# Kernel tuning notes

Measured on AMD Instinct MI355X. Metric: run time of the kernel, lower is better.

Reference implementation:

```python
import jax, jax.numpy as jnp
import numpy as np

D_MODEL = 768
EXPAND = 2
D_INNER = EXPAND * D_MODEL  # 1536
D_STATE = 16
D_CONV = 4
DT_RANK = D_MODEL // 16  # 48
N_LAYER = 3
BATCH, SEQLEN = 2, 1024
EPS = 1e-5


def setup_inputs() -> dict:
    key = jax.random.key(0)
    ks = jax.random.split(key, 8)
    s = 0.02
    hidden_states = jax.random.normal(ks[0], (BATCH, SEQLEN, D_MODEL), jnp.float32)
    norm_w = jnp.ones((N_LAYER, D_MODEL), jnp.float32)
    in_proj_w = s * jax.random.normal(ks[1], (N_LAYER, 2 * D_INNER, D_MODEL), jnp.float32)
    conv_w = s * jax.random.normal(ks[2], (N_LAYER, D_INNER, D_CONV), jnp.float32)
    conv_b = jnp.zeros((N_LAYER, D_INNER), jnp.float32)
    x_proj_w = s * jax.random.normal(ks[3], (N_LAYER, DT_RANK + 2 * D_STATE, D_INNER), jnp.float32)
    dt_proj_w = s * jax.random.normal(ks[4], (N_LAYER, D_INNER, DT_RANK), jnp.float32)
    dt_proj_b = jnp.full((N_LAYER, D_INNER), -4.6, jnp.float32)  # softplus ~ 0.01
    # S4D-real init: A_log = log(1..d_state), tiled over channels
    A_log = jnp.tile(jnp.log(jnp.arange(1, D_STATE + 1, dtype=jnp.float32))[None, None, :], (N_LAYER, D_INNER, 1))
    D_skip = jnp.ones((N_LAYER, D_INNER), jnp.float32)
    out_proj_w = s * jax.random.normal(ks[5], (N_LAYER, D_MODEL, D_INNER), jnp.float32)
    norm_f_w = jnp.ones((D_MODEL,), jnp.float32)
    return dict(hidden_states=hidden_states, norm_w=norm_w, in_proj_w=in_proj_w,
                conv_w=conv_w, conv_b=conv_b, x_proj_w=x_proj_w, dt_proj_w=dt_proj_w,
                dt_proj_b=dt_proj_b, A_log=A_log, D_skip=D_skip, out_proj_w=out_proj_w,
                norm_f_w=norm_f_w)


def _rmsnorm(x, w):
    return x * jax.lax.rsqrt(jnp.mean(x * x, axis=-1, keepdims=True) + EPS) * w


def _causal_conv1d(x, w, b):
    # x: [B, L, D]; w: [D, K] depthwise; left-pad for causality
    xt = jnp.transpose(x, (0, 2, 1))  # [B, D, L]
    y = jax.lax.conv_general_dilated(xt, w[:, None, :], window_strides=(1,),
                                     padding=[(D_CONV - 1, 0)], feature_group_count=D_INNER)
    return jnp.transpose(y, (0, 2, 1)) + b


def _selective_scan(u, delta, A, Bc, Cc, Dp):
    # u, delta: [B, L, D]; A: [D, N]; Bc, Cc: [B, L, N]
    def step(h, inp):
        dt, bt, ct, ut = inp  # [B,D], [B,N], [B,N], [B,D]
        h = jnp.exp(dt[..., None] * A) * h + (dt * ut)[..., None] * bt[:, None, :]
        y = jnp.einsum('bdn,bn->bd', h, ct)
        return h, y
    h0 = jnp.zeros((u.shape[0], u.shape[2], A.shape[1]), u.dtype)
    xs = (jnp.swapaxes(delta, 0, 1), jnp.swapaxes(Bc, 0, 1), jnp.swapaxes(Cc, 0, 1), jnp.swapaxes(u, 0, 1))
    _, ys = jax.lax.scan(step, h0, xs)  # ys: [L, B, D]
    return jnp.swapaxes(ys, 0, 1) + u * Dp


def _mixer(h, in_w, cw, cb, xw, dtw, dtb, A_log, Dp, ow):
    xz = jnp.einsum('bld,ed->ble', h, in_w)  # [B, L, 2*D_INNER]
    x, z = xz[..., :D_INNER], xz[..., D_INNER:]
    x = jax.nn.silu(_causal_conv1d(x, cw, cb))
    x_dbl = jnp.einsum('bld,ed->ble', x, xw)
    dt = x_dbl[..., :DT_RANK]
    Bc = x_dbl[..., DT_RANK:DT_RANK + D_STATE]
    Cc = x_dbl[..., DT_RANK + D_STATE:]
    delta = jax.nn.softplus(jnp.einsum('blr,dr->bld', dt, dtw) + dtb)
    A = -jnp.exp(A_log)
    y = _selective_scan(x, delta, A, Bc, Cc, Dp)
    y = y * jax.nn.silu(z)
    return jnp.einsum('bld,ed->ble', y, ow)


def reference(hidden_states, norm_w, in_proj_w, conv_w, conv_b, x_proj_w, dt_proj_w,
              dt_proj_b, A_log, D_skip, out_proj_w, norm_f_w):
    hidden = hidden_states
    residual = None
    for i in range(N_LAYER):
        residual = hidden if residual is None else hidden + residual  # fused add
        hidden = _rmsnorm(residual, norm_w[i])
        hidden = _mixer(hidden, in_proj_w[i], conv_w[i], conv_b[i], x_proj_w[i],
                        dt_proj_w[i], dt_proj_b[i], A_log[i], D_skip[i], out_proj_w[i])
    # final fused add + RMSNorm (prenorm=False)
    return _rmsnorm(hidden + residual, norm_f_w)
```

## Files before the change

### kernel.cpp

```cpp
#include <hip/hip_runtime.h>
#include <math.h>

#define D_MODEL 768
#define D_INNER 1536
#define D_STATE 16
#define D_CONV 4
#define DT_RANK 48
#define N_LAYER 3
#define BATCH 2
#define SEQLEN 1024
#define NROWS (BATCH * SEQLEN)
#define XDBL_W (DT_RANK + 2 * D_STATE)
#define EPS 1e-5f

#define SCLEN 16
#define SDN 16
#define KSPLIT_X 8

typedef short bf16x8 __attribute__((ext_vector_type(8)));
typedef float f32x4 __attribute__((ext_vector_type(4)));

__device__ __forceinline__ ushort f2bf(float x) {
    union { float f; uint u; } v; v.f = x;
    uint r = v.u + 0x7fff + ((v.u >> 16) & 1);
    return (ushort)(r >> 16);
}

__device__ __forceinline__ void gload_lds16(const void* g, void* l) {
    __builtin_amdgcn_global_load_lds(
        (const __attribute__((address_space(1))) unsigned int*)g,
        (__attribute__((address_space(3))) unsigned int*)l, 16, 0, 0);
}

__global__ __launch_bounds__(256) void cvt_bf16_kernel(
    const float* __restrict__ s, ushort* __restrict__ d, int n4)
{
    int i = blockIdx.x * 256 + threadIdx.x;
    if (i >= n4) return;
    float4 v = ((const float4*)s)[i];
    ushort4 o;
    o.x = f2bf(v.x); o.y = f2bf(v.y); o.z = f2bf(v.z); o.w = f2bf(v.w);
    ((ushort4*)d)[i] = o;
}

__global__ __launch_bounds__(256) void cvt_xw_pad_kernel(
    const float* __restrict__ src, ushort* __restrict__ dst)
{
    const int per = 128 * 1536 / 4;
    int i = blockIdx.x * 256 + threadIdx.x;
    if (i >= 3 * per) return;
    int li = i / per, rem = i - li * per;
    int r = (rem * 4) / 1536, c = (rem * 4) % 1536;
    ushort4 o = make_ushort4(0, 0, 0, 0);
    if (r < XDBL_W) {
        const float* s = src + ((size_t)li * XDBL_W + r) * 1536 + c;
        o.x = f2bf(s[0]); o.y = f2bf(s[1]); o.z = f2bf(s[2]); o.w = f2bf(s[3]);
    }
    ((ushort4*)dst)[i] = o;
}

__global__ __launch_bounds__(256) void cvt_dtw_pad_kernel(
    const float* __restrict__ src, ushort* __restrict__ dst)
{
    const int per = 1536 * 64 / 4;
    int i = blockIdx.x * 256 + threadIdx.x;
    if (i >= 3 * per) return;
    int li = i / per, rem = i - li * per;
    int r = (rem * 4) / 64, c = (rem * 4) % 64;
    ushort4 o = make_ushort4(0, 0, 0, 0);
    if (c < DT_RANK) {
        const float* s = src + ((size_t)li * 1536 + r) * DT_RANK + c;
        o.x = f2bf(s[0]); o.y = f2bf(s[1]); o.z = f2bf(s[2]); o.w = f2bf(s[3]);
    }
    ((ushort4*)dst)[i] = o;
}

__global__ __launch_bounds__(256) void add_rmsnorm_kernel(
    const float* __restrict__ x, const float* __restrict__ res_in,
    const float* __restrict__ w, float* __restrict__ res_out,
    float* __restrict__ normed_f32, ushort* __restrict__ normed_bf)
{
    int row = blockIdx.x;
    int tid = threadIdx.x;
    const float* xr = x + row * D_MODEL;
    float v[3];
    float ss = 0.f;
#pragma unroll
    for (int i = 0; i < 3; i++) {
        int c = tid + i * 256;
        float t = xr[c];
        if (res_in) t += res_in[row * D_MODEL + c];
        v[i] = t;
        ss += t * t;
    }
    for (int off = 32; off; off >>= 1) ss += __shfl_xor(ss, off, 64);
    __shared__ float red[4];
    if ((tid & 63) == 0) red[tid >> 6] = ss;
    __syncthreads();
    float tot = red[0] + red[1] + red[2] + red[3];
    float scale = rsqrtf(tot * (1.f / D_MODEL) + EPS);
#pragma unroll
    for (int i = 0; i < 3; i++) {
        int c = tid + i * 256;
        if (res_out) res_out[row * D_MODEL + c] = v[i];
        float o = v[i] * scale * w[c];
        if (normed_f32) normed_f32[row * D_MODEL + c] = o;
        if (normed_bf)  normed_bf[row * D_MODEL + c] = f2bf(o);
    }
}

template <int BM, int BN, int EPI, int SPLITK>
__global__ __launch_bounds__(256) void gemm_mfma_kernel(
    const ushort* __restrict__ A, const ushort* __restrict__ W,
    const float* __restrict__ bias, float* __restrict__ C,
    int ldc, int Nout, int M, int K)
{
    constexpr int TM = BM / 32;
    constexpr int TN = BN / 32;
    __shared__ __attribute__((aligned(16))) ushort As[BM * 64];
    __shared__ __attribute__((aligned(16))) ushort Ws[BN * 64];
    const int t = threadIdx.x;
    const int lane = t & 63, w = t >> 6;
    const int ln15 = lane & 15, q = lane >> 4;
    const int row0 = blockIdx.y * BM, col0 = blockIdx.x * BN;
    const int wm0 = (w & 1) * (BM / 2), wn0 = (w >> 1) * (BN / 2);

    int kper = K / SPLITK;
    int kz = (SPLITK > 1) ? blockIdx.z * kper : 0;
    if (SPLITK > 1) C += (size_t)blockIdx.z * M * ldc;

    f32x4 acc[TM][TN];
#pragma unroll
    for (int i = 0; i < TM; i++)
#pragma unroll
        for (int j = 0; j < TN; j++) acc[i][j] = (f32x4){0.f, 0.f, 0.f, 0.f};

    for (int k0 = kz; k0 < kz + kper; k0 += 64) {
        __syncthreads();
#pragma unroll
        for (int i = 0; i < BM / 32; i++) {
            int p = (i * 4 + w) * 64 + lane;
            int r = p >> 3, s = p & 7;
            int g = s ^ (r & 7);
            gload_lds16(A + (size_t)(row0 + r) * K + k0 + g * 8, &As[p * 8]);
        }
#pragma unroll
        for (int i = 0; i < BN / 32; i++) {
            int p = (i * 4 + w) * 64 + lane;
            int r = p >> 3, s = p & 7;
            int g = s ^ (r & 7);
            gload_lds16(W + (size_t)(col0 + r) * K + k0 + g * 8, &Ws[p * 8]);
        }
        __syncthreads();
#pragma unroll
        for (int ks = 0; ks < 2; ks++) {
            bf16x8 af[TM], wf[TN];
#pragma unroll
            for (int im = 0; im < TM; im++) {
                int m = wm0 + im * 16 + ln15;
                int slot = (ks * 4 + q) ^ (m & 7);
                af[im] = *(const bf16x8*)&As[m * 64 + slot * 8];
            }
#pragma unroll
            for (int jn = 0; jn < TN; jn++) {
                int n = wn0 + jn * 16 + ln15;
                int slot = (ks * 4 + q) ^ (n & 7);
                wf[jn] = *(const bf16x8*)&Ws[n * 64 + slot * 8];
            }
#pragma unroll
            for (int im = 0; im < TM; im++)
#pragma unroll
                for (int jn = 0; jn < TN; jn++)
                    acc[im][jn] = __builtin_amdgcn_mfma_f32_16x16x32_bf16(
                        af[im], wf[jn], acc[im][jn], 0, 0, 0);
        }
    }
#pragma unroll
    for (int im = 0; im < TM; im++) {
#pragma unroll
        for (int jn = 0; jn < TN; jn++) {
            int rr = row0 + wm0 + im * 16 + q * 4;
            int cc = col0 + wn0 + jn * 16 + ln15;
            if (cc < Nout) {
                float* cp = C + (size_t)rr * ldc + cc;
#pragma unroll
                for (int r = 0; r < 4; r++) {
                    float v = acc[im][jn][r];
                    if (EPI == 1) {
                        v += bias[cc];
                        v = (v > 20.f) ? v : log1pf(__expf(v));
                    }
                    cp[(size_t)r * ldc] = v;
                }
            }
        }
    }
}

__global__ __launch_bounds__(256) void xreduce_kernel(
    const float* __restrict__ Cp, float* __restrict__ xdbl,
    ushort* __restrict__ xdt)
{
    const int S4 = NROWS * XDBL_W / 4;
    int i = blockIdx.x * 256 + threadIdx.x;
    if (i >= S4) return;
    const float4* p = (const float4*)Cp;
    float4 o = p[i];
#pragma unroll
    for (int z = 1; z < KSPLIT_X; z++) {
        float4 a = p[i + (size_t)z * S4];
        o.x += a.x; o.y += a.y; o.z += a.z; o.w += a.w;
    }
    ((float4*)xdbl)[i] = o;
    int row = (i * 4) / XDBL_W, c0 = (i * 4) % XDBL_W;
    if (c0 < DT_RANK) {
        ushort4 b;
        b.x = f2bf(o.x); b.y = f2bf(o.y); b.z = f2bf(o.z); b.w = f2bf(o.w);
        *(ushort4*)&xdt[(size_t)row * 64 + c0] = b;
    } else if (c0 < 64) {
        *(ushort4*)&xdt[(size_t)row * 64 + c0] = make_ushort4(0, 0, 0, 0);
    }
}

__global__ __launch_bounds__(256) void conv_silu_kernel(
    const float* __restrict__ xz, const float* __restrict__ cw,
    const float* __restrict__ cb, float* __restrict__ out,
    ushort* __restrict__ out_bf)
{
    int idx = blockIdx.x * 256 + threadIdx.x;
    int d = idx % D_INNER;
    int bl = idx / D_INNER;
    int l = bl % SEQLEN;
    float s = cb[d];
    const float* xp = xz + (size_t)bl * (2 * D_INNER) + d;
#pragma unroll
    for (int k = 0; k < D_CONV; k++) {
        int ls = l - (D_CONV - 1) + k;
        if (ls >= 0) s += cw[d * D_CONV + k] * xp[(k - (D_CONV - 1)) * (2 * D_INNER)];
    }
    float sil = s / (1.f + __expf(-s));
    out[(size_t)bl * D_INNER + d] = sil;
    out_bf[(size_t)bl * D_INNER + d] = f2bf(sil);
}

__global__ __launch_bounds__(1024) void scan2_kernel(
    const float* __restrict__ u, const float* __restrict__ delta,
    const float* __restrict__ A_log, const float* __restrict__ xdbl,
    const float* __restrict__ Dskip, const float* __restrict__ xz,
    ushort* __restrict__ ybf)
{
    __shared__ float PL[16][SDN * 17];
    __shared__ float HL[16][SDN * 17];
    const int t = threadIdx.x;
    const int lane = t & 63;
    const int w = t >> 6;
    const int dsub = lane & 15;
    const int csub = lane >> 4;
    const int c = w * 4 + csub;
    const int b = blockIdx.x / (D_INNER / SDN);
    const int d = (blockIdx.x % (D_INNER / SDN)) * SDN + dsub;

    float a2[D_STATE];
#pragma unroll
    for (int n = 0; n < D_STATE; n++)
        a2[n] = -__expf(A_log[d * D_STATE + n]) * 1.44269504f;

    const size_t base = (size_t)b * SEQLEN * D_INNER + d;
    const float* dtp = delta + base;
    const float* up  = u + base;
    const float* xrow = xdbl + (size_t)b * SEQLEN * XDBL_W;
    const int l0 = c * SCLEN;

    float h[D_STATE], P[D_STATE];
#pragma unroll
    for (int n = 0; n < D_STATE; n++) { h[n] = 0.f; P[n] = 1.f; }

    for (int i = 0; i < SCLEN; i++) {
        const int l = l0 + i;
        float dt = dtp[(size_t)l * D_INNER];
        float uu = up[(size_t)l * D_INNER];
        const float4* Bv = (const float4*)(xrow + (size_t)l * XDBL_W + DT_RANK);
        float4 q0 = Bv[0], q1 = Bv[1], q2 = Bv[2], q3 = Bv[3];
        float Bf[D_STATE] = {q0.x,q0.y,q0.z,q0.w, q1.x,q1.y,q1.z,q1.w,
                             q2.x,q2.y,q2.z,q2.w, q3.x,q3.y,q3.z,q3.w};
        float dtu = dt * uu;
#pragma unroll
        for (int n = 0; n < D_STATE; n++) {
            float e = __builtin_amdgcn_exp2f(dt * a2[n]);
            P[n] *= e;
            h[n] = e * h[n] + dtu * Bf[n];
        }
    }

#pragma unroll
    for (int n = 0; n < D_STATE; n++) {
        float Pp = __shfl(P[n], lane - 16, 64);
        float Hp = __shfl(h[n], lane - 16, 64);
        bool act = csub >= 1;
        h[n] = act ? P[n] * Hp + h[n] : h[n];
        P[n] = act ? P[n] * Pp : P[n];
    }
#pragma unroll
    for (int n = 0; n < D_STATE; n++) {
        float Pp = __shfl(P[n], lane - 32, 64);
        float Hp = __shfl(h[n], lane - 32, 64);
        bool act = csub >= 2;
        h[n] = act ? P[n] * Hp + h[n] : h[n];
        P[n] = act ? P[n] * Pp : P[n];
    }

    if (csub == 3) {
#pragma unroll
        for (int n = 0; n < D_STATE; n++) {
            PL[w][dsub * 17 + n] = P[n];
            HL[w][dsub * 17 + n] = h[n];
        }
    }
    __syncthreads();

    if (t < SDN * D_STATE) {
        const int d2 = t >> 4, n2 = t & 15;
        float hin = 0.f;
        for (int ww = 0; ww < 16; ww++) {
            float Pw = PL[ww][d2 * 17 + n2];
            float Hw = HL[ww][d2 * 17 + n2];
            HL[ww][d2 * 17 + n2] = hin;
            hin = Pw * hin + Hw;
        }
    }
    __syncthreads();

#pragma unroll
    for (int n = 0; n < D_STATE; n++) {
        float Win = HL[w][dsub * 17 + n];
        float Pe = __shfl(P[n], lane - 16, 64);
        float He = __shfl(h[n], lane - 16, 64);
        h[n] = (csub == 0) ? Win : Pe * Win + He;
    }

    const float Dsk = Dskip[d];
    const float* zp = xz + (size_t)b * SEQLEN * (2 * D_INNER) + D_INNER + d;
    ushort* yp = ybf + base;
    for (int i = 0; i < SCLEN; i++) {
        const int l = l0 + i;
        float dt = dtp[(size_t)l * D_INNER];
        float uu = up[(size_t)l * D_INNER];
        float zz = zp[(size_t)l * (2 * D_INNER)];
        const float4* Bv = (const float4*)(xrow + (size_t)l * XDBL_W + DT_RANK);
        float4 q0 = Bv[0], q1 = Bv[1], q2 = Bv[2], q3 = Bv[3];
        float4 r0 = Bv[4], r1 = Bv[5], r2 = Bv[6], r3 = Bv[7];
        float Bf[D_STATE] = {q0.x,q0.y,q0.z,q0.w, q1.x,q1.y,q1.z,q1.w,
                             q2.x,q2.y,q2.z,q2.w, q3.x,q3.y,q3.z,q3.w};
        float Cf[D_STATE] = {r0.x,r0.y,r0.z,r0.w, r1.x,r1.y,r1.z,r1.w,
                             r2.x,r2.y,r2.z,r2.w, r3.x,r3.y,r3.z,r3.w};
        float dtu = dt * uu;
        float acc = 0.f;
#pragma unroll
        for (int n = 0; n < D_STATE; n++) {
            float e = __builtin_amdgcn_exp2f(dt * a2[n]);
            h[n] = e * h[n] + dtu * Bf[n];
            acc += h[n] * Cf[n];
        }
        float yy = acc + uu * Dsk;
        float ee = __builtin_amdgcn_exp2f(-zz * 1.44269504f);
        float sil = zz * __builtin_amdgcn_rcpf(1.f + ee);
        yp[(size_t)l * D_INNER] = f2bf(yy * sil);
    }
}

extern "C" void kernel_launch(void* const* d_in, const int* in_sizes, int n_in,
                              void* d_out, int out_size, void* d_ws, size_t ws_size,
                              hipStream_t stream)
{
    const float* hs        = (const float*)d_in[0];
    const float* norm_w    = (const float*)d_in[1];
    const float* in_proj_w = (const float*)d_in[2];
    const float* conv_w    = (const float*)d_in[3];
    const float* conv_b    = (const float*)d_in[4];
    const float* x_proj_w  = (const float*)d_in[5];
    const float* dt_proj_w = (const float*)d_in[6];
    const float* dt_proj_b = (const float*)d_in[7];
    const float* A_log     = (const float*)d_in[8];
    const float* D_skip    = (const float*)d_in[9];
    const float* out_proj_w= (const float*)d_in[10];
    const float* norm_f_w  = (const float*)d_in[11];

    float* ws = (float*)d_ws;
    float* residual = ws;
    float* hidden   = residual + NROWS * D_MODEL;
    float* xz       = hidden + NROWS * D_MODEL;
    float* xconv    = xz + NROWS * 2 * D_INNER;
    float* xdbl     = xconv + NROWS * D_INNER;
    float* delta    = xdbl + NROWS * XDBL_W;
    float* xpart    = delta + NROWS * D_INNER;
    ushort* normbf  = (ushort*)(xpart + (size_t)KSPLIT_X * NROWS * XDBL_W);
    ushort* ybf     = normbf + NROWS * D_MODEL;
    ushort* xconvbf = ybf + NROWS * D_INNER;
    ushort* xdtbf   = xconvbf + NROWS * D_INNER;
    ushort* win_bf  = xdtbf + NROWS * 64;
    ushort* wout_bf = win_bf + (size_t)N_LAYER * 2 * D_INNER * D_MODEL;
    ushort* xw_pad  = wout_bf + (size_t)N_LAYER * D_MODEL * D_INNER;
    ushort* dtw_pad = xw_pad + (size_t)N_LAYER * 128 * 1536;

    {
        int n_in4  = N_LAYER * 2 * D_INNER * D_MODEL / 4;
        int n_out4 = N_LAYER * D_MODEL * D_INNER / 4;
        cvt_bf16_kernel<<<(n_in4 + 255) / 256, 256, 0, stream>>>(in_proj_w, win_bf, n_in4);
        cvt_bf16_kernel<<<(n_out4 + 255) / 256, 256, 0, stream>>>(out_proj_w, wout_bf, n_out4);
        cvt_xw_pad_kernel<<<(3 * 128 * 1536 / 4 + 255) / 256, 256, 0, stream>>>(x_proj_w, xw_pad);
        cvt_dtw_pad_kernel<<<(3 * 1536 * 64 / 4 + 255) / 256, 256, 0, stream>>>(dt_proj_w, dtw_pad);
    }

    for (int i = 0; i < N_LAYER; i++) {
        add_rmsnorm_kernel<<<NROWS, 256, 0, stream>>>(
            i == 0 ? hs : hidden, i == 0 ? nullptr : residual,
            norm_w + i * D_MODEL, residual, nullptr, normbf);
        gemm_mfma_kernel<64, 128, 0, 1><<<dim3(2 * D_INNER / 128, NROWS / 64), 256, 0, stream>>>(
            normbf, win_bf + (size_t)i * 2 * D_INNER * D_MODEL, nullptr,
            xz, 2 * D_INNER, 2 * D_INNER, NROWS, D_MODEL);
        conv_silu_kernel<<<NROWS * D_INNER / 256, 256, 0, stream>>>(
            xz, conv_w + i * D_INNER * D_CONV, conv_b + i * D_INNER, xconv, xconvbf);
        gemm_mfma_kernel<64, 128, 0, KSPLIT_X><<<dim3(1, NROWS / 64, KSPLIT_X), 256, 0, stream>>>(
            xconvbf, xw_pad + (size_t)i * 128 * 1536, nullptr,
            xpart, XDBL_W, XDBL_W, NROWS, D_INNER);
        xreduce_kernel<<<(NROWS * XDBL_W / 4 + 255) / 256, 256, 0, stream>>>(
            xpart, xdbl, xdtbf);
        gemm_mfma_kernel<128, 128, 1, 1><<<dim3(D_INNER / 128, NROWS / 128), 256, 0, stream>>>(
            xdtbf, dtw_pad + (size_t)i * 1536 * 64, dt_proj_b + i * D_INNER,
            delta, D_INNER, D_INNER, NROWS, 64);
        scan2_kernel<<<BATCH * (D_INNER / SDN), 1024, 0, stream>>>(
            xconv, delta, A_log + (size_t)i * D_INNER * D_STATE, xdbl,
            D_skip + i * D_INNER, xz, ybf);
        gemm_mfma_kernel<64, 64, 0, 1><<<dim3(D_MODEL / 64, NROWS / 64), 256, 0, stream>>>(
            ybf, wout_bf + (size_t)i * D_MODEL * D_INNER, nullptr,
            hidden, D_MODEL, D_MODEL, NROWS, D_INNER);
    }
    add_rmsnorm_kernel<<<NROWS, 256, 0, stream>>>(
        hidden, residual, norm_f_w, nullptr, (float*)d_out, nullptr);
}
```

Before: 498.7 us.

## Store scan inputs channel-major so the scan reads contiguous float4 chunks

The z half of in_proj and the dt_proj GEMM are computed with swapped operands so they write transposed [D_INNER, NROWS] outputs. A new tiled conv+SiLU kernel transposes u through shared memory into the same layout. The scan kernel then loads each chunk's delta, u and z as contiguous float4 vectors into registers instead of doing strided per-timestep loads. It also replaces the running product P with a single exp2 of the summed dt. The cost is an extra GEMM launch, a shared-memory transpose step, and new bias-per-row epilogue logic.

Measured after the change: 852.6 us. +71.0%, slower.

```diff
diff --git a/kernel.cpp b/kernel.cpp
--- a/kernel.cpp
+++ b/kernel.cpp
@@ -189,6 +189,9 @@
                     if (EPI == 1) {
                         v += bias[cc];
                         v = (v > 20.f) ? v : log1pf(__expf(v));
+                    } else if (EPI == 2) {
+                        v += bias[rr + r];
+                        v = (v > 20.f) ? v : log1pf(__expf(v));
                     }
                     cp[(size_t)r * ldc] = v;
                 }
@@ -222,31 +225,55 @@
     }
 }
 
-__global__ __launch_bounds__(256) void conv_silu_kernel(
-    const float* __restrict__ xz, const float* __restrict__ cw,
-    const float* __restrict__ cb, float* __restrict__ out,
-    ushort* __restrict__ out_bf)
-{
-    int idx = blockIdx.x * 256 + threadIdx.x;
-    int d = idx % D_INNER;
-    int bl = idx / D_INNER;
-    int l = bl % SEQLEN;
-    float s = cb[d];
-    const float* xp = xz + (size_t)bl * (2 * D_INNER) + d;
-#pragma unroll
-    for (int k = 0; k < D_CONV; k++) {
-        int ls = l - (D_CONV - 1) + k;
-        if (ls >= 0) s += cw[d * D_CONV + k] * xp[(k - (D_CONV - 1)) * (2 * D_INNER)];
-    }
-    float sil = s / (1.f + __expf(-s));
-    out[(size_t)bl * D_INNER + d] = sil;
-    out_bf[(size_t)bl * D_INNER + d] = f2bf(sil);
+__global__ __launch_bounds__(256) void conv_silu_t_kernel(
+    const float* __restrict__ xz_x, const float* __restrict__ cw,
+    const float* __restrict__ cb, ushort* __restrict__ out_bf,
+    float* __restrict__ u_T)
+{
+    __shared__ float XT[68][64];
+    __shared__ float YT[64][65];
+    const int l0 = blockIdx.x * 64;
+    const int d0 = blockIdx.y * 64;
+    const int b  = blockIdx.z;
+    const int t  = threadIdx.x;
+
+    for (int i = t; i < 67 * 64; i += 256) {
+        int r = i >> 6, cc = i & 63;
+        int gl = l0 - 3 + r;
+        XT[r][cc] = (gl >= 0)
+            ? xz_x[((size_t)b * SEQLEN + gl) * D_INNER + d0 + cc] : 0.f;
+    }
+    __syncthreads();
+
+    const int dloc = t & 63, lg = t >> 6;
+    const int d = d0 + dloc;
+    const float w0 = cw[d * D_CONV + 0], w1 = cw[d * D_CONV + 1];
+    const float w2 = cw[d * D_CONV + 2], w3 = cw[d * D_CONV + 3];
+    const float bb = cb[d];
+#pragma unroll
+    for (int i = 0; i < 16; i++) {
+        int l = lg * 16 + i;
+        float s = bb + w0 * XT[l][dloc] + w1 * XT[l + 1][dloc]
+                     + w2 * XT[l + 2][dloc] + w3 * XT[l + 3][dloc];
+        float sil = s / (1.f + __expf(-s));
+        out_bf[((size_t)b * SEQLEN + l0 + l) * D_INNER + d] = f2bf(sil);
+        YT[dloc][l] = sil;
+    }
+    __syncthreads();
+
+    const int lloc = t & 63, dg = t >> 6;
+#pragma unroll
+    for (int i = 0; i < 16; i++) {
+        int dd = dg * 16 + i;
+        u_T[((size_t)(d0 + dd)) * NROWS + (size_t)b * SEQLEN + l0 + lloc] =
+            YT[dd][lloc];
+    }
 }
 
 __global__ __launch_bounds__(1024) void scan2_kernel(
-    const float* __restrict__ u, const float* __restrict__ delta,
+    const float* __restrict__ u_T, const float* __restrict__ delta_T,
     const float* __restrict__ A_log, const float* __restrict__ xdbl,
-    const float* __restrict__ Dskip, const float* __restrict__ xz,
+    const float* __restrict__ Dskip, const float* __restrict__ z_T,
     ushort* __restrict__ ybf)
 {
     __shared__ float PL[16][SDN * 17];
@@ -265,32 +292,47 @@
     for (int n = 0; n < D_STATE; n++)
         a2[n] = -__expf(A_log[d * D_STATE + n]) * 1.44269504f;
 
-    const size_t base = (size_t)b * SEQLEN * D_INNER + d;
-    const float* dtp = delta + base;
-    const float* up  = u + base;
+    const int l0 = c * SCLEN;
+    const size_t col = (size_t)b * SEQLEN + l0;
+    const float* dtp = delta_T + (size_t)d * NROWS + col;
+    const float* up  = u_T     + (size_t)d * NROWS + col;
+    const float* zp  = z_T     + (size_t)d * NROWS + col;
     const float* xrow = xdbl + (size_t)b * SEQLEN * XDBL_W;
-    const int l0 = c * SCLEN;
-
-    float h[D_STATE], P[D_STATE];
-#pragma unroll
-    for (int n = 0; n < D_STATE; n++) { h[n] = 0.f; P[n] = 1.f; }
-
+
+    float dtv[SCLEN], uv[SCLEN];
+#pragma unroll
+    for (int j = 0; j < 4; j++) {
+        float4 a = ((const float4*)dtp)[j];
+        float4 g = ((const float4*)up)[j];
+        dtv[j*4+0]=a.x; dtv[j*4+1]=a.y; dtv[j*4+2]=a.z; dtv[j*4+3]=a.w;
+        uv [j*4+0]=g.x; uv [j*4+1]=g.y; uv [j*4+2]=g.z; uv [j*4+3]=g.w;
+    }
+
+    float h[D_STATE];
+#pragma unroll
+    for (int n = 0; n < D_STATE; n++) h[n] = 0.f;
+    float sdt = 0.f;
+
+#pragma unroll
     for (int i = 0; i < SCLEN; i++) {
         const int l = l0 + i;
-        float dt = dtp[(size_t)l * D_INNER];
-        float uu = up[(size_t)l * D_INNER];
+        float dt = dtv[i];
+        float dtu = dt * uv[i];
+        sdt += dt;
         const float4* Bv = (const float4*)(xrow + (size_t)l * XDBL_W + DT_RANK);
         float4 q0 = Bv[0], q1 = Bv[1], q2 = Bv[2], q3 = Bv[3];
         float Bf[D_STATE] = {q0.x,q0.y,q0.z,q0.w, q1.x,q1.y,q1.z,q1.w,
                              q2.x,q2.y,q2.z,q2.w, q3.x,q3.y,q3.z,q3.w};
-        float dtu = dt * uu;
 #pragma unroll
         for (int n = 0; n < D_STATE; n++) {
             float e = __builtin_amdgcn_exp2f(dt * a2[n]);
-            P[n] *= e;
             h[n] = e * h[n] + dtu * Bf[n];
         }
     }
+    float P[D_STATE];
+#pragma unroll
+    for (int n = 0; n < D_STATE; n++)
+        P[n] = __builtin_amdgcn_exp2f(a2[n] * sdt);
 
 #pragma unroll
     for (int n = 0; n < D_STATE; n++) {
@@ -338,14 +380,20 @@
         h[n] = (csub == 0) ? Win : Pe * Win + He;
     }
 
+    float zv[SCLEN];
+#pragma unroll
+    for (int j = 0; j < 4; j++) {
+        float4 g = ((const float4*)up)[j];
+        float4 zq = ((const float4*)zp)[j];
+        uv[j*4+0]=g.x; uv[j*4+1]=g.y; uv[j*4+2]=g.z; uv[j*4+3]=g.w;
+        zv[j*4+0]=zq.x; zv[j*4+1]=zq.y; zv[j*4+2]=zq.z; zv[j*4+3]=zq.w;
+    }
     const float Dsk = Dskip[d];
-    const float* zp = xz + (size_t)b * SEQLEN * (2 * D_INNER) + D_INNER + d;
-    ushort* yp = ybf + base;
+    ushort* yp = ybf + (size_t)b * SEQLEN * D_INNER + d;
+#pragma unroll
     for (int i = 0; i < SCLEN; i++) {
         const int l = l0 + i;
-        float dt = dtp[(size_t)l * D_INNER];
-        float uu = up[(size_t)l * D_INNER];
-        float zz = zp[(size_t)l * (2 * D_INNER)];
+        float dt = dtv[i], uu = uv[i], zz = zv[i];
         const float4* Bv = (const float4*)(xrow + (size_t)l * XDBL_W + DT_RANK);
         float4 q0 = Bv[0], q1 = Bv[1], q2 = Bv[2], q3 = Bv[3];
         float4 r0 = Bv[4], r1 = Bv[5], r2 = Bv[6], r3 = Bv[7];
@@ -388,11 +436,12 @@
     float* ws = (float*)d_ws;
     float* residual = ws;
     float* hidden   = residual + NROWS * D_MODEL;
-    float* xz       = hidden + NROWS * D_MODEL;
-    float* xconv    = xz + NROWS * 2 * D_INNER;
-    float* xdbl     = xconv + NROWS * D_INNER;
-    float* delta    = xdbl + NROWS * XDBL_W;
-    float* xpart    = delta + NROWS * D_INNER;
+    float* xz_x     = hidden + NROWS * D_MODEL;
+    float* z_T      = xz_x + (size_t)NROWS * D_INNER;
+    float* u_T      = z_T + (size_t)D_INNER * NROWS;
+    float* xdbl     = u_T + (size_t)D_INNER * NROWS;
+    float* delta_T  = xdbl + NROWS * XDBL_W;
+    float* xpart    = delta_T + (size_t)D_INNER * NROWS;
     ushort* normbf  = (ushort*)(xpart + (size_t)KSPLIT_X * NROWS * XDBL_W);
     ushort* ybf     = normbf + NROWS * D_MODEL;
     ushort* xconvbf = ybf + NROWS * D_INNER;
@@ -412,25 +461,29 @@
     }
 
     for (int i = 0; i < N_LAYER; i++) {
+        const ushort* win_x = win_bf + (size_t)i * 2 * D_INNER * D_MODEL;
+        const ushort* win_z = win_x + (size_t)D_INNER * D_MODEL;
         add_rmsnorm_kernel<<<NROWS, 256, 0, stream>>>(
             i == 0 ? hs : hidden, i == 0 ? nullptr : residual,
             norm_w + i * D_MODEL, residual, nullptr, normbf);
-        gemm_mfma_kernel<64, 128, 0, 1><<<dim3(2 * D_INNER / 128, NROWS / 64), 256, 0, stream>>>(
-            normbf, win_bf + (size_t)i * 2 * D_INNER * D_MODEL, nullptr,
-            xz, 2 * D_INNER, 2 * D_INNER, NROWS, D_MODEL);
-        conv_silu_kernel<<<NROWS * D_INNER / 256, 256, 0, stream>>>(
-            xz, conv_w + i * D_INNER * D_CONV, conv_b + i * D_INNER, xconv, xconvbf);
+        gemm_mfma_kernel<64, 128, 0, 1><<<dim3(D_INNER / 128, NROWS / 64), 256, 0, stream>>>(
+            normbf, win_x, nullptr, xz_x, D_INNER, D_INNER, NROWS, D_MODEL);
+        gemm_mfma_kernel<64, 128, 0, 1><<<dim3(NROWS / 128, D_INNER / 64), 256, 0, stream>>>(
+            win_z, normbf, nullptr, z_T, NROWS, NROWS, D_INNER, D_MODEL);
+        conv_silu_t_kernel<<<dim3(SEQLEN / 64, D_INNER / 64, BATCH), 256, 0, stream>>>(
+            xz_x, conv_w + i * D_INNER * D_CONV, conv_b + i * D_INNER,
+            xconvbf, u_T);
         gemm_mfma_kernel<64, 128, 0, KSPLIT_X><<<dim3(1, NROWS / 64, KSPLIT_X), 256, 0, stream>>>(
             xconvbf, xw_pad + (size_t)i * 128 * 1536, nullptr,
             xpart, XDBL_W, XDBL_W, NROWS, D_INNER);
         xreduce_kernel<<<(NROWS * XDBL_W / 4 + 255) / 256, 256, 0, stream>>>(
             xpart, xdbl, xdtbf);
-        gemm_mfma_kernel<128, 128, 1, 1><<<dim3(D_INNER / 128, NROWS / 128), 256, 0, stream>>>(
-            xdtbf, dtw_pad + (size_t)i * 1536 * 64, dt_proj_b + i * D_INNER,
-            delta, D_INNER, D_INNER, NROWS, 64);
+        gemm_mfma_kernel<64, 128, 2, 1><<<dim3(NROWS / 128, D_INNER / 64), 256, 0, stream>>>(
+            dtw_pad + (size_t)i * 1536 * 64, xdtbf, dt_proj_b + i * D_INNER,
+            delta_T, NROWS, NROWS, D_INNER, 64);
         scan2_kernel<<<BATCH * (D_INNER / SDN), 1024, 0, stream>>>(
-            xconv, delta, A_log + (size_t)i * D_INNER * D_STATE, xdbl,
-            D_skip + i * D_INNER, xz, ybf);
+            u_T, delta_T, A_log + (size_t)i * D_INNER * D_STATE, xdbl,
+            D_skip + i * D_INNER, z_T, ybf);
         gemm_mfma_kernel<64, 64, 0, 1><<<dim3(D_MODEL / 64, NROWS / 64), 256, 0, stream>>>(
             ybf, wout_bf + (size_t)i * D_MODEL * D_INNER, nullptr,
             hidden, D_MODEL, D_MODEL, NROWS, D_INNER);
```
